# Optimization experiments

Hardware: AMD Instinct MI355X
Metric: run time of the kernel (lower is better)

## Reference

```python
import jax, jax.numpy as jnp
import numpy as np

S = 8192          # past KV length
H = 4096          # hidden size
NH = 32           # heads
HD = 128          # head dim
INNER = 16384     # MLP inner (4h)
ROT = 64          # rotary dim per 2D-rope half
NUM_LAYERS = 28
LAYER_ID = 0
ALPHA = (2.0 * NUM_LAYERS) ** 0.5
QK_COEFF = float(LAYER_ID + 1)            # query_key_layer_scaling_coeff
COEFF = (128.0 ** 0.5) * QK_COEFF         # math.sqrt(128) * coeff
EPS = 1e-5


def layernorm(x, w, b):
    mu = jnp.mean(x, axis=-1, keepdims=True)
    var = jnp.var(x, axis=-1, keepdims=True)
    return (x - mu) * jax.lax.rsqrt(var + EPS) * w + b


def rotate_half(x):
    # x: [..., 64]; GLM rotate-half at 32
    return jnp.concatenate([-x[..., 32:], x[..., :32]], axis=-1)


def setup_inputs() -> dict:
    key = jax.random.key(0)
    ks = jax.random.split(key, 16)
    # rotary cache (as in the driver script)
    inv_freq = 1.0 / (10000.0 ** (jnp.arange(0, ROT, 2, dtype=jnp.float32) / ROT))  # [32]
    t = jnp.arange(512, dtype=jnp.float32)
    freqs = jnp.einsum('i,j->ij', t, inv_freq)          # [512,32]
    emb = jnp.concatenate([freqs, freqs], axis=-1)      # [512,64]
    w = lambda k, shp: jax.random.normal(k, shp, dtype=jnp.float32) * 0.02
    return {
        'hidden_states': jax.random.normal(ks[0], (1, H), dtype=jnp.float32),
        'past_key': jax.random.normal(ks[1], (S, NH, HD), dtype=jnp.float32),
        'past_value': jax.random.normal(ks[2], (S, NH, HD), dtype=jnp.float32),
        'cos_cached': jnp.cos(emb),
        'sin_cached': jnp.sin(emb),
        'ln1_w': jnp.ones((H,), jnp.float32), 'ln1_b': jnp.zeros((H,), jnp.float32),
        'qkv_w': w(ks[3], (3 * H, H)), 'qkv_b': w(ks[4], (3 * H,)),
        'dense_w': w(ks[5], (H, H)), 'dense_b': w(ks[6], (H,)),
        'ln2_w': jnp.ones((H,), jnp.float32), 'ln2_b': jnp.zeros((H,), jnp.float32),
        'fc1_w': w(ks[7], (INNER, H)), 'fc1_b': w(ks[8], (INNER,)),
        'fc2_w': w(ks[9], (H, INNER)), 'fc2_b': w(ks[10], (H,)),
        'position_ids': jax.random.randint(ks[11], (1, 1), 0, 512),
        'block_position_ids': jax.random.randint(ks[12], (1, 1), 0, 512),
        'attention_mask': jnp.zeros((1, 1, S + 1), dtype=bool),
    }


def reference(hidden_states, past_key, past_value, cos_cached, sin_cached,
              ln1_w, ln1_b, qkv_w, qkv_b, dense_w, dense_b,
              ln2_w, ln2_b, fc1_w, fc1_b, fc2_w, fc2_b,
              position_ids, block_position_ids, attention_mask):
    # rotary lookups: embedding then transpose(0,1) -> [q_len,1,64]
    pos_cos = jnp.transpose(cos_cached[position_ids], (1, 0, 2))
    pos_sin = jnp.transpose(sin_cached[position_ids], (1, 0, 2))
    blk_cos = jnp.transpose(cos_cached[block_position_ids], (1, 0, 2))
    blk_sin = jnp.transpose(sin_cached[block_position_ids], (1, 0, 2))

    residual = layernorm(hidden_states, ln1_w, ln1_b)          # [1, H]
    qkv = residual @ qkv_w.T + qkv_b                           # [1, 3H]
    qkv = qkv.reshape(-1, NH, 3 * HD)                          # [1, 32, 384]
    query, key_new, value_new = jnp.split(qkv, 3, axis=2)      # each [1,32,128]

    q1, q2 = jnp.split(query, 2, axis=2)                       # [1,32,64] each
    k1, k2 = jnp.split(key_new, 2, axis=2)
    q1 = q1 * pos_cos + rotate_half(q1) * pos_sin
    k1 = k1 * pos_cos + rotate_half(k1) * pos_sin
    q2 = q2 * blk_cos + rotate_half(q2) * blk_sin
    k2 = k2 * blk_cos + rotate_half(k2) * blk_sin
    q = jnp.concatenate([q1, q2], axis=-1)                     # [1,32,128]
    k_new = jnp.concatenate([k1, k2], axis=-1)                 # [1,32,128]

    k = jnp.concatenate([past_key, k_new], axis=0)             # [S+1,32,128]
    v = jnp.concatenate([past_value, value_new], axis=0)       # [S+1,32,128]

    # scores: [heads, q=1, S+1]
    scores = jnp.einsum('qhd,khd->hqk', q / COEFF, k)
    scores = jnp.where(attention_mask, jnp.float32(-10000.0), scores)
    scores = scores * QK_COEFF
    probs = jax.nn.softmax(scores, axis=-1)
    ctx = jnp.einsum('hqk,khd->qhd', probs, v).reshape(-1, H)  # [1,4096]

    attn_out = ctx @ dense_w.T + dense_b
    hidden = residual * ALPHA + attn_out

    residual2 = layernorm(hidden, ln2_w, ln2_b)
    mlp = jax.nn.gelu(residual2 @ fc1_w.T + fc1_b, approximate=True)
    mlp = mlp @ fc2_w.T + fc2_b
    out = residual2 * ALPHA + mlp
    return (out, k, v)
```

## Files before the change

### kernel.cpp

```cpp
#include <hip/hip_runtime.h>
#include <math.h>

#define S_PAST 8192
#define S_TOT  8193
#define HID    4096
#define NH     32
#define HD     128
#define INNER  16384
#define CH     32
#define NCH    257
#define S_PAD  (NCH * CH)
#define ALPHA_ 7.483314773547883f
#define INV_COEFF 0.08838834764831845f
#define EPS_ 1e-5f

__global__ __launch_bounds__(256) void ln_kernel(const float* __restrict__ xin,
                                                 const float* __restrict__ w,
                                                 const float* __restrict__ b,
                                                 float* __restrict__ out) {
    int tid = threadIdx.x;
    float xs[16];
    float s = 0.f, s2 = 0.f;
#pragma unroll
    for (int i = 0; i < 16; ++i) {
        float v = xin[tid + i * 256];
        xs[i] = v; s += v; s2 += v * v;
    }
    for (int off = 32; off; off >>= 1) {
        s  += __shfl_down(s, off, 64);
        s2 += __shfl_down(s2, off, 64);
    }
    __shared__ float rs[4], rs2[4];
    __shared__ float mu_s, ri_s;
    int wid = tid >> 6, lane = tid & 63;
    if (lane == 0) { rs[wid] = s; rs2[wid] = s2; }
    __syncthreads();
    if (tid == 0) {
        float S1 = rs[0] + rs[1] + rs[2] + rs[3];
        float S2 = rs2[0] + rs2[1] + rs2[2] + rs2[3];
        float mu = S1 / HID;
        float var = S2 / HID - mu * mu;
        mu_s = mu;
        ri_s = rsqrtf(var + EPS_);
    }
    __syncthreads();
    float mu = mu_s, ri = ri_s;
#pragma unroll
    for (int i = 0; i < 16; ++i) {
        int idx = tid + i * 256;
        out[idx] = (xs[i] - mu) * ri * w[idx] + b[idx];
    }
}

template <int C, int MODE>
__global__ __launch_bounds__(256) void gemv_kernel(
        const float* __restrict__ Wm, const float* __restrict__ bias,
        const float* __restrict__ x, float* __restrict__ y,
        const float* __restrict__ res) {
    int wid = threadIdx.x >> 6, lane = threadIdx.x & 63;
    int r = blockIdx.x * 4 + wid;
    const float4* __restrict__ rowv = (const float4*)(Wm + (size_t)r * C);
    const float4* __restrict__ xv = (const float4*)x;
    constexpr int IT = C / 4 / 64;
    float acc0 = 0.f, acc1 = 0.f;
#pragma unroll
    for (int it = 0; it < IT; it += 2) {
        float4 w0 = rowv[lane + it * 64];
        float4 x0 = xv[lane + it * 64];
        float4 w1 = rowv[lane + (it + 1) * 64];
        float4 x1 = xv[lane + (it + 1) * 64];
        acc0 += w0.x * x0.x + w0.y * x0.y + w0.z * x0.z + w0.w * x0.w;
        acc1 += w1.x * x1.x + w1.y * x1.y + w1.z * x1.z + w1.w * x1.w;
    }
    float acc = acc0 + acc1;
    for (int off = 32; off; off >>= 1) acc += __shfl_down(acc, off, 64);
    if (lane == 0) {
        float t = acc + bias[r];
        if (MODE == 1) t += ALPHA_ * res[r];
        if (MODE == 2) {
            float u = t;
            t = 0.5f * u * (1.f + tanhf(0.7978845608028654f * (u + 0.044715f * u * u * u)));
        }
        y[r] = t;
    }
}

__global__ __launch_bounds__(128) void rope_kv_kernel(
        const float* __restrict__ qkv, const float* __restrict__ cosc,
        const float* __restrict__ sinc, const int* __restrict__ pos_ids,
        const int* __restrict__ blk_ids, float* __restrict__ qrot,
        float* __restrict__ kout, float* __restrict__ vout) {
    int h = blockIdx.x, d = threadIdx.x;
    int pos = pos_ids[0], blk = blk_ids[0];
    const float* qh = qkv + h * 384;
    float q = qh[d], k = qh[128 + d], v = qh[256 + d];
    int half = d >> 6;
    int i = d & 63;
    int p = half ? blk : pos;
    float c = cosc[p * 64 + i];
    float s = sinc[p * 64 + i];
    float qpart, kpart;
    int base = half * 64;
    if (i < 32) { qpart = -qh[base + i + 32]; kpart = -qh[128 + base + i + 32]; }
    else        { qpart =  qh[base + i - 32]; kpart =  qh[128 + base + i - 32]; }
    float qo = q * c + qpart * s;
    float ko = k * c + kpart * s;
    qrot[h * HD + d] = qo * INV_COEFF;
    size_t o = (size_t)S_PAST * HID + h * HD + d;
    kout[o] = ko;
    vout[o] = v;
}

__global__ __launch_bounds__(256) void scores_kcopy(
        const float* __restrict__ qrot, const float* __restrict__ pastk,
        float* __restrict__ kout, const unsigned char* __restrict__ mask,
        float* __restrict__ scores) {
    int tid = threadIdx.x;
    int s0 = blockIdx.x * CH;
    const float4* __restrict__ qv = (const float4*)qrot;
    float4 q0 = qv[tid * 4 + 0], q1 = qv[tid * 4 + 1];
    float4 q2 = qv[tid * 4 + 2], q3 = qv[tid * 4 + 3];
    __shared__ float sc[CH][NH + 1];
#pragma unroll 4
    for (int r = 0; r < CH; ++r) {
        int srow = s0 + r;
        float dot = 0.f;
        if (srow < S_TOT) {
            const float* kbase = (srow < S_PAST) ? pastk : kout;
            const float4* krow = (const float4*)(kbase + (size_t)srow * HID);
            float4 k0 = krow[tid * 4 + 0], k1 = krow[tid * 4 + 1];
            float4 k2 = krow[tid * 4 + 2], k3 = krow[tid * 4 + 3];
            if (srow < S_PAST) {
                float4* ko = (float4*)(kout + (size_t)srow * HID);
                ko[tid * 4 + 0] = k0; ko[tid * 4 + 1] = k1;
                ko[tid * 4 + 2] = k2; ko[tid * 4 + 3] = k3;
            }
            dot = q0.x * k0.x + q0.y * k0.y + q0.z * k0.z + q0.w * k0.w
                + q1.x * k1.x + q1.y * k1.y + q1.z * k1.z + q1.w * k1.w
                + q2.x * k2.x + q2.y * k2.y + q2.z * k2.z + q2.w * k2.w
                + q3.x * k3.x + q3.y * k3.y + q3.z * k3.z + q3.w * k3.w;
        }
        dot += __shfl_xor(dot, 1, 64);
        dot += __shfl_xor(dot, 2, 64);
        dot += __shfl_xor(dot, 4, 64);
        if ((tid & 7) == 0) sc[r][tid >> 3] = dot;
    }
    __syncthreads();
    for (int i = tid; i < CH * NH; i += 256) {
        int r = i & (CH - 1), h = i >> 5;
        int srow = s0 + r;
        float v;
        if (srow >= S_TOT) v = -1e30f;
        else v = mask[srow] ? -10000.f : sc[r][h];
        scores[(size_t)h * S_PAD + s0 + r] = v;
    }
}

__global__ __launch_bounds__(256) void softmax_kernel(float* __restrict__ scores) {
    int h = blockIdx.x, tid = threadIdx.x;
    float* row = scores + (size_t)h * S_PAD;
    float m = -1e30f;
    for (int i = tid; i < S_PAD; i += 256) m = fmaxf(m, row[i]);
    for (int off = 32; off; off >>= 1) m = fmaxf(m, __shfl_down(m, off, 64));
    __shared__ float wm[4], wl[4];
    __shared__ float Ms, Ls;
    int wid = tid >> 6, lane = tid & 63;
    if (lane == 0) wm[wid] = m;
    __syncthreads();
    if (tid == 0) Ms = fmaxf(fmaxf(wm[0], wm[1]), fmaxf(wm[2], wm[3]));
    __syncthreads();
    float M = Ms;
    float l = 0.f;
    for (int i = tid; i < S_PAD; i += 256) l += __expf(row[i] - M);
    for (int off = 32; off; off >>= 1) l += __shfl_down(l, off, 64);
    if (lane == 0) wl[wid] = l;
    __syncthreads();
    if (tid == 0) Ls = wl[0] + wl[1] + wl[2] + wl[3];
    __syncthreads();
    float inv = 1.f / Ls;
    for (int i = tid; i < S_PAD; i += 256) row[i] = __expf(row[i] - M) * inv;
}

__global__ __launch_bounds__(256) void pv_vcopy(
        const float* __restrict__ probs, const float* __restrict__ pastv,
        float* __restrict__ vout, float* __restrict__ pctx) {
    int tid = threadIdx.x;
    int s0 = blockIdx.x * CH;
    __shared__ float pl[NH][CH + 1];
    for (int i = tid; i < NH * CH; i += 256) {
        int h = i >> 5, r = i & (CH - 1);
        pl[h][r] = probs[(size_t)h * S_PAD + s0 + r];
    }
    __syncthreads();
    int h = tid >> 3;
    float4 a0 = {0,0,0,0}, a1 = {0,0,0,0}, a2 = {0,0,0,0}, a3 = {0,0,0,0};
#pragma unroll 4
    for (int r = 0; r < CH; ++r) {
        int srow = s0 + r;
        if (srow >= S_TOT) break;
        const float* vbase = (srow < S_PAST) ? pastv : vout;
        const float4* vrow = (const float4*)(vbase + (size_t)srow * HID);
        float4 v0 = vrow[tid * 4 + 0], v1 = vrow[tid * 4 + 1];
        float4 v2 = vrow[tid * 4 + 2], v3 = vrow[tid * 4 + 3];
        if (srow < S_PAST) {
            float4* vo = (float4*)(vout + (size_t)srow * HID);
            vo[tid * 4 + 0] = v0; vo[tid * 4 + 1] = v1;
            vo[tid * 4 + 2] = v2; vo[tid * 4 + 3] = v3;
        }
        float p = pl[h][r];
        a0.x += p * v0.x; a0.y += p * v0.y; a0.z += p * v0.z; a0.w += p * v0.w;
        a1.x += p * v1.x; a1.y += p * v1.y; a1.z += p * v1.z; a1.w += p * v1.w;
        a2.x += p * v2.x; a2.y += p * v2.y; a2.z += p * v2.z; a2.w += p * v2.w;
        a3.x += p * v3.x; a3.y += p * v3.y; a3.z += p * v3.z; a3.w += p * v3.w;
    }
    float4* pc = (float4*)(pctx + (size_t)blockIdx.x * HID);
    pc[tid * 4 + 0] = a0; pc[tid * 4 + 1] = a1;
    pc[tid * 4 + 2] = a2; pc[tid * 4 + 3] = a3;
}

__global__ __launch_bounds__(256) void ctx_combine(const float* __restrict__ pctx,
                                                   float* __restrict__ ctx) {
    int idx = blockIdx.x * 256 + threadIdx.x;
    float a = 0.f;
    for (int c = 0; c < NCH; ++c) a += pctx[(size_t)c * HID + idx];
    ctx[idx] = a;
}

extern "C" void kernel_launch(void* const* d_in, const int* in_sizes, int n_in,
                              void* d_out, int out_size, void* d_ws, size_t ws_size,
                              hipStream_t stream) {
    const float* hidden = (const float*)d_in[0];
    const float* past_k = (const float*)d_in[1];
    const float* past_v = (const float*)d_in[2];
    const float* cosc = (const float*)d_in[3];
    const float* sinc = (const float*)d_in[4];
    const float* ln1w = (const float*)d_in[5];
    const float* ln1b = (const float*)d_in[6];
    const float* qkvw = (const float*)d_in[7];
    const float* qkvb = (const float*)d_in[8];
    const float* denw = (const float*)d_in[9];
    const float* denb = (const float*)d_in[10];
    const float* ln2w = (const float*)d_in[11];
    const float* ln2b = (const float*)d_in[12];
    const float* fc1w = (const float*)d_in[13];
    const float* fc1b = (const float*)d_in[14];
    const float* fc2w = (const float*)d_in[15];
    const float* fc2b = (const float*)d_in[16];
    const int* pos = (const int*)d_in[17];
    const int* blk = (const int*)d_in[18];
    const unsigned char* mask = (const unsigned char*)d_in[19];

    float* out_f = (float*)d_out;
    float* kout = out_f + HID;
    float* vout = kout + (size_t)S_TOT * HID;

    float* ws = (float*)d_ws;
    float* resid1 = ws;
    float* qkvv   = ws + 4096;
    float* qrot   = ws + 16384;
    float* ctx    = ws + 20480;
    float* hid2   = ws + 24576;
    float* resid2 = ws + 28672;
    float* mlpi   = ws + 32768;
    float* scores = ws + 49152;
    float* pctx   = ws + 49152 + NH * S_PAD;

    ln_kernel<<<1, 256, 0, stream>>>(hidden, ln1w, ln1b, resid1);
    gemv_kernel<HID, 0><<<3 * HID / 4, 256, 0, stream>>>(qkvw, qkvb, resid1, qkvv, nullptr);
    rope_kv_kernel<<<NH, HD, 0, stream>>>(qkvv, cosc, sinc, pos, blk, qrot, kout, vout);
    scores_kcopy<<<NCH, 256, 0, stream>>>(qrot, past_k, kout, mask, scores);
    softmax_kernel<<<NH, 256, 0, stream>>>(scores);
    pv_vcopy<<<NCH, 256, 0, stream>>>(scores, past_v, vout, pctx);
    ctx_combine<<<16, 256, 0, stream>>>(pctx, ctx);
    gemv_kernel<HID, 1><<<HID / 4, 256, 0, stream>>>(denw, denb, ctx, hid2, resid1);
    ln_kernel<<<1, 256, 0, stream>>>(hid2, ln2w, ln2b, resid2);
    gemv_kernel<HID, 2><<<INNER / 4, 256, 0, stream>>>(fc1w, fc1b, resid2, mlpi, nullptr);
    gemv_kernel<INNER, 1><<<HID / 4, 256, 0, stream>>>(fc2w, fc2b, mlpi, out_f, resid2);
}
```

Before: 341.5 us.

## Fuse per-chunk softmax stats into scores kernel and normalize inside PV

The scores kernel now computes per-chunk max and exp-sum per head, and a small combine kernel reduces these to a global max and inverse sum per head. The PV kernel applies exp and normalization on the fly, so the full softmax pass that read the score matrix twice and wrote it back is gone. The thread-to-element mapping also switches to strided float4 access, so a wavefront's loads and stores for a K/V row are contiguous. This adds shuffle reductions across 32 lanes per row instead of 8.

```diff
diff --git a/kernel.cpp b/kernel.cpp
--- a/kernel.cpp
+++ b/kernel.cpp
@@ -114,56 +114,76 @@
 __global__ __launch_bounds__(256) void scores_kcopy(
         const float* __restrict__ qrot, const float* __restrict__ pastk,
         float* __restrict__ kout, const unsigned char* __restrict__ mask,
-        float* __restrict__ scores) {
+        float* __restrict__ scores, float* __restrict__ pm, float* __restrict__ pe) {
     int tid = threadIdx.x;
     int s0 = blockIdx.x * CH;
+    int a = tid >> 5;
     const float4* __restrict__ qv = (const float4*)qrot;
-    float4 q0 = qv[tid * 4 + 0], q1 = qv[tid * 4 + 1];
-    float4 q2 = qv[tid * 4 + 2], q3 = qv[tid * 4 + 3];
+    float4 q0 = qv[tid], q1 = qv[256 + tid], q2 = qv[512 + tid], q3 = qv[768 + tid];
     __shared__ float sc[CH][NH + 1];
 #pragma unroll 4
     for (int r = 0; r < CH; ++r) {
         int srow = s0 + r;
-        float dot = 0.f;
+        float d0 = -1e30f, d1 = 0.f, d2 = 0.f, d3 = 0.f;
         if (srow < S_TOT) {
             const float* kbase = (srow < S_PAST) ? pastk : kout;
             const float4* krow = (const float4*)(kbase + (size_t)srow * HID);
-            float4 k0 = krow[tid * 4 + 0], k1 = krow[tid * 4 + 1];
-            float4 k2 = krow[tid * 4 + 2], k3 = krow[tid * 4 + 3];
+            float4 k0 = krow[tid], k1 = krow[256 + tid];
+            float4 k2 = krow[512 + tid], k3 = krow[768 + tid];
             if (srow < S_PAST) {
                 float4* ko = (float4*)(kout + (size_t)srow * HID);
-                ko[tid * 4 + 0] = k0; ko[tid * 4 + 1] = k1;
-                ko[tid * 4 + 2] = k2; ko[tid * 4 + 3] = k3;
+                ko[tid] = k0; ko[256 + tid] = k1; ko[512 + tid] = k2; ko[768 + tid] = k3;
             }
-            dot = q0.x * k0.x + q0.y * k0.y + q0.z * k0.z + q0.w * k0.w
-                + q1.x * k1.x + q1.y * k1.y + q1.z * k1.z + q1.w * k1.w
-                + q2.x * k2.x + q2.y * k2.y + q2.z * k2.z + q2.w * k2.w
-                + q3.x * k3.x + q3.y * k3.y + q3.z * k3.z + q3.w * k3.w;
-        }
-        dot += __shfl_xor(dot, 1, 64);
-        dot += __shfl_xor(dot, 2, 64);
-        dot += __shfl_xor(dot, 4, 64);
-        if ((tid & 7) == 0) sc[r][tid >> 3] = dot;
+            d0 = q0.x * k0.x + q0.y * k0.y + q0.z * k0.z + q0.w * k0.w;
+            d1 = q1.x * k1.x + q1.y * k1.y + q1.z * k1.z + q1.w * k1.w;
+            d2 = q2.x * k2.x + q2.y * k2.y + q2.z * k2.z + q2.w * k2.w;
+            d3 = q3.x * k3.x + q3.y * k3.y + q3.z * k3.z + q3.w * k3.w;
+        }
+#pragma unroll
+        for (int off = 1; off < 32; off <<= 1) {
+            d0 += __shfl_xor(d0, off, 64);
+            d1 += __shfl_xor(d1, off, 64);
+            d2 += __shfl_xor(d2, off, 64);
+            d3 += __shfl_xor(d3, off, 64);
+        }
+        if ((tid & 31) == 0) {
+            float v0, v1, v2, v3;
+            if (srow >= S_TOT) { v0 = v1 = v2 = v3 = -1e30f; }
+            else if (mask[srow]) { v0 = v1 = v2 = v3 = -10000.f; }
+            else { v0 = d0; v1 = d1; v2 = d2; v3 = d3; }
+            sc[r][a] = v0; sc[r][8 + a] = v1; sc[r][16 + a] = v2; sc[r][24 + a] = v3;
+        }
     }
     __syncthreads();
     for (int i = tid; i < CH * NH; i += 256) {
         int r = i & (CH - 1), h = i >> 5;
-        int srow = s0 + r;
-        float v;
-        if (srow >= S_TOT) v = -1e30f;
-        else v = mask[srow] ? -10000.f : sc[r][h];
-        scores[(size_t)h * S_PAD + s0 + r] = v;
-    }
-}
-
-__global__ __launch_bounds__(256) void softmax_kernel(float* __restrict__ scores) {
+        scores[(size_t)h * S_PAD + s0 + r] = sc[r][h];
+    }
+    int h = tid >> 3, j = tid & 7;
+    if (tid < 256) {
+        float m = -1e30f;
+#pragma unroll
+        for (int k = 0; k < 4; ++k) m = fmaxf(m, sc[j + 8 * k][h]);
+#pragma unroll
+        for (int off = 1; off < 8; off <<= 1) m = fmaxf(m, __shfl_xor(m, off, 64));
+        float e = 0.f;
+#pragma unroll
+        for (int k = 0; k < 4; ++k) e += __expf(sc[j + 8 * k][h] - m);
+#pragma unroll
+        for (int off = 1; off < 8; off <<= 1) e += __shfl_xor(e, off, 64);
+        if (j == 0) { pm[h * NCH + blockIdx.x] = m; pe[h * NCH + blockIdx.x] = e; }
+    }
+}
+
+__global__ __launch_bounds__(256) void ml_combine(
+        const float* __restrict__ pm, const float* __restrict__ pe,
+        float* __restrict__ Mh, float* __restrict__ iLh) {
     int h = blockIdx.x, tid = threadIdx.x;
-    float* row = scores + (size_t)h * S_PAD;
     float m = -1e30f;
-    for (int i = tid; i < S_PAD; i += 256) m = fmaxf(m, row[i]);
+    for (int c = tid; c < NCH; c += 256) m = fmaxf(m, pm[h * NCH + c]);
     for (int off = 32; off; off >>= 1) m = fmaxf(m, __shfl_down(m, off, 64));
     __shared__ float wm[4], wl[4];
-    __shared__ float Ms, Ls;
+    __shared__ float Ms;
     int wid = tid >> 6, lane = tid & 63;
     if (lane == 0) wm[wid] = m;
     __syncthreads();
@@ -171,28 +191,26 @@
     __syncthreads();
     float M = Ms;
     float l = 0.f;
-    for (int i = tid; i < S_PAD; i += 256) l += __expf(row[i] - M);
+    for (int c = tid; c < NCH; c += 256) l += pe[h * NCH + c] * __expf(pm[h * NCH + c] - M);
     for (int off = 32; off; off >>= 1) l += __shfl_down(l, off, 64);
     if (lane == 0) wl[wid] = l;
     __syncthreads();
-    if (tid == 0) Ls = wl[0] + wl[1] + wl[2] + wl[3];
-    __syncthreads();
-    float inv = 1.f / Ls;
-    for (int i = tid; i < S_PAD; i += 256) row[i] = __expf(row[i] - M) * inv;
+    if (tid == 0) { Mh[h] = M; iLh[h] = 1.f / (wl[0] + wl[1] + wl[2] + wl[3]); }
 }
 
 __global__ __launch_bounds__(256) void pv_vcopy(
-        const float* __restrict__ probs, const float* __restrict__ pastv,
+        const float* __restrict__ scores, const float* __restrict__ Mh,
+        const float* __restrict__ iLh, const float* __restrict__ pastv,
         float* __restrict__ vout, float* __restrict__ pctx) {
     int tid = threadIdx.x;
     int s0 = blockIdx.x * CH;
+    int a = tid >> 5;
     __shared__ float pl[NH][CH + 1];
     for (int i = tid; i < NH * CH; i += 256) {
         int h = i >> 5, r = i & (CH - 1);
-        pl[h][r] = probs[(size_t)h * S_PAD + s0 + r];
-    }
-    __syncthreads();
-    int h = tid >> 3;
+        pl[h][r] = __expf(scores[(size_t)h * S_PAD + s0 + r] - Mh[h]) * iLh[h];
+    }
+    __syncthreads();
     float4 a0 = {0,0,0,0}, a1 = {0,0,0,0}, a2 = {0,0,0,0}, a3 = {0,0,0,0};
 #pragma unroll 4
     for (int r = 0; r < CH; ++r) {
@@ -200,22 +218,20 @@
         if (srow >= S_TOT) break;
         const float* vbase = (srow < S_PAST) ? pastv : vout;
         const float4* vrow = (const float4*)(vbase + (size_t)srow * HID);
-        float4 v0 = vrow[tid * 4 + 0], v1 = vrow[tid * 4 + 1];
-        float4 v2 = vrow[tid * 4 + 2], v3 = vrow[tid * 4 + 3];
+        float4 v0 = vrow[tid], v1 = vrow[256 + tid];
+        float4 v2 = vrow[512 + tid], v3 = vrow[768 + tid];
         if (srow < S_PAST) {
             float4* vo = (float4*)(vout + (size_t)srow * HID);
-            vo[tid * 4 + 0] = v0; vo[tid * 4 + 1] = v1;
-            vo[tid * 4 + 2] = v2; vo[tid * 4 + 3] = v3;
-        }
-        float p = pl[h][r];
-        a0.x += p * v0.x; a0.y += p * v0.y; a0.z += p * v0.z; a0.w += p * v0.w;
-        a1.x += p * v1.x; a1.y += p * v1.y; a1.z += p * v1.z; a1.w += p * v1.w;
-        a2.x += p * v2.x; a2.y += p * v2.y; a2.z += p * v2.z; a2.w += p * v2.w;
-        a3.x += p * v3.x; a3.y += p * v3.y; a3.z += p * v3.z; a3.w += p * v3.w;
+            vo[tid] = v0; vo[256 + tid] = v1; vo[512 + tid] = v2; vo[768 + tid] = v3;
+        }
+        float p0 = pl[a][r], p1 = pl[8 + a][r], p2 = pl[16 + a][r], p3 = pl[24 + a][r];
+        a0.x += p0 * v0.x; a0.y += p0 * v0.y; a0.z += p0 * v0.z; a0.w += p0 * v0.w;
+        a1.x += p1 * v1.x; a1.y += p1 * v1.y; a1.z += p1 * v1.z; a1.w += p1 * v1.w;
+        a2.x += p2 * v2.x; a2.y += p2 * v2.y; a2.z += p2 * v2.z; a2.w += p2 * v2.w;
+        a3.x += p3 * v3.x; a3.y += p3 * v3.y; a3.z += p3 * v3.z; a3.w += p3 * v3.w;
     }
     float4* pc = (float4*)(pctx + (size_t)blockIdx.x * HID);
-    pc[tid * 4 + 0] = a0; pc[tid * 4 + 1] = a1;
-    pc[tid * 4 + 2] = a2; pc[tid * 4 + 3] = a3;
+    pc[tid] = a0; pc[256 + tid] = a1; pc[512 + tid] = a2; pc[768 + tid] = a3;
 }
 
 __global__ __launch_bounds__(256) void ctx_combine(const float* __restrict__ pctx,
@@ -263,14 +279,18 @@
     float* resid2 = ws + 28672;
     float* mlpi   = ws + 32768;
     float* scores = ws + 49152;
-    float* pctx   = ws + 49152 + NH * S_PAD;
+    float* pm     = ws + 312320;
+    float* pe     = ws + 320544;
+    float* Mh     = ws + 328768;
+    float* iLh    = ws + 328800;
+    float* pctx   = ws + 328832;
 
     ln_kernel<<<1, 256, 0, stream>>>(hidden, ln1w, ln1b, resid1);
     gemv_kernel<HID, 0><<<3 * HID / 4, 256, 0, stream>>>(qkvw, qkvb, resid1, qkvv, nullptr);
     rope_kv_kernel<<<NH, HD, 0, stream>>>(qkvv, cosc, sinc, pos, blk, qrot, kout, vout);
-    scores_kcopy<<<NCH, 256, 0, stream>>>(qrot, past_k, kout, mask, scores);
-    softmax_kernel<<<NH, 256, 0, stream>>>(scores);
-    pv_vcopy<<<NCH, 256, 0, stream>>>(scores, past_v, vout, pctx);
+    scores_kcopy<<<NCH, 256, 0, stream>>>(qrot, past_k, kout, mask, scores, pm, pe);
+    ml_combine<<<NH, 256, 0, stream>>>(pm, pe, Mh, iLh);
+    pv_vcopy<<<NCH, 256, 0, stream>>>(scores, Mh, iLh, past_v, vout, pctx);
     ctx_combine<<<16, 256, 0, stream>>>(pctx, ctx);
     gemv_kernel<HID, 1><<<HID / 4, 256, 0, stream>>>(denw, denb, ctx, hid2, resid1);
     ln_kernel<<<1, 256, 0, stream>>>(hid2, ln2w, ln2b, resid2);
```

Result: faster. 327.6 us (-4.1%).
